# Optimization experiments

Measured on AMD Instinct MI355X. Metric: run time of the kernel, lower is better.

## Reference

```python
import jax, jax.numpy as jnp
import numpy as np

D = 128        # d_model
VOCAB = 2000   # vocab_size
NUM_ITERS = 6
NUM_V = 98304  # total vertices = 3 * num_edges
NUM_E = NUM_V // 3


def setup_inputs() -> dict:
    key = jax.random.key(0)
    ks = jax.random.split(key, 20)
    std = 0.02
    inp = {
        "x_v": jax.random.randint(ks[0], (NUM_V,), 0, VOCAB),
        "target_mask": jax.random.randint(ks[1], (NUM_V,), 0, 2) > 0,
        # embedding table (vocab_size + 1 rows, last is padding idx)
        "emb": jax.random.normal(ks[2], (VOCAB + 1, D), jnp.float32) * std,
        # edge_init: Linear(1, d_model)
        "edge_init_w": jax.random.normal(ks[3], (D, 1), jnp.float32) * std,
        "edge_init_b": jnp.zeros((D,), jnp.float32),
        # vertex_to_edge LSTM(3d -> d): torch gate order i,f,g,o
        "Wih_v2e": jax.random.normal(ks[4], (4 * D, 3 * D), jnp.float32) * (1.0 / np.sqrt(D)),
        "Whh_v2e": jax.random.normal(ks[5], (4 * D, D), jnp.float32) * (1.0 / np.sqrt(D)),
        "bih_v2e": jax.random.normal(ks[6], (4 * D,), jnp.float32) * (1.0 / np.sqrt(D)),
        "bhh_v2e": jax.random.normal(ks[7], (4 * D,), jnp.float32) * (1.0 / np.sqrt(D)),
        # edge_to_vertex: 3 position-specific LSTM(d -> d), stacked along axis 0
        "Wih_e2v": jax.random.normal(ks[8], (3, 4 * D, D), jnp.float32) * (1.0 / np.sqrt(D)),
        "Whh_e2v": jax.random.normal(ks[9], (3, 4 * D, D), jnp.float32) * (1.0 / np.sqrt(D)),
        "bih_e2v": jax.random.normal(ks[10], (3, 4 * D), jnp.float32) * (1.0 / np.sqrt(D)),
        "bhh_e2v": jax.random.normal(ks[11], (3, 4 * D), jnp.float32) * (1.0 / np.sqrt(D)),
        # output projection Linear(d -> vocab)
        "out_w": jax.random.normal(ks[12], (VOCAB, D), jnp.float32) * std,
        "out_b": jnp.zeros((VOCAB,), jnp.float32),
    }
    return inp


def _lstm_cell(gates, c):
    # torch LSTM gate order: input, forget, cell(g), output
    i, f, g, o = jnp.split(gates, 4, axis=-1)
    c_new = jax.nn.sigmoid(f) * c + jax.nn.sigmoid(i) * jnp.tanh(g)
    h_new = jax.nn.sigmoid(o) * jnp.tanh(c_new)
    return h_new, c_new


def reference(x_v, target_mask, emb, edge_init_w, edge_init_b,
              Wih_v2e, Whh_v2e, bih_v2e, bhh_v2e,
              Wih_e2v, Whh_e2v, bih_e2v, bhh_e2v,
              out_w, out_b):
    E = x_v.shape[0] // 3
    # init embeddings (-1 ids would map to padding row VOCAB; ids are in-range here)
    h_v = emb[x_v].reshape(E, 3, D)              # [E, 3, D]
    c_v = jnp.zeros_like(h_v)
    h_e = jnp.broadcast_to(edge_init_w[:, 0] + edge_init_b, (E, D))  # Linear(1->D) on ones
    c_e = jnp.zeros_like(h_e)
    mask = target_mask.reshape(E, 3)[..., None]  # [E, 3, 1]
    b_v2e = bih_v2e + bhh_v2e                    # [4D]
    b_e2v = (bih_e2v + bhh_e2v)[None]            # [1, 3, 4D]

    for _ in range(NUM_ITERS):
        # vertex -> edge: concat 3 vertices, one LSTM cell step
        msg = h_v.reshape(E, 3 * D)
        gates_e = msg @ Wih_v2e.T + h_e @ Whh_v2e.T + b_v2e          # [E, 4D]
        h_e, c_e = _lstm_cell(gates_e, c_e)
        # edge -> vertex: 3 position-specific LSTM cells, same edge input
        gates_v = (jnp.einsum('ed,pkd->epk', h_e, Wih_e2v)
                   + jnp.einsum('epd,pkd->epk', h_v, Whh_e2v)
                   + b_e2v)                                          # [E, 3, 4D]
        h_new, c_new = _lstm_cell(gates_v, c_v)
        h_v = jnp.where(mask, h_new, h_v)
        c_v = jnp.where(mask, c_new, c_v)

    logits = h_v.reshape(3 * E, D) @ out_w.T + out_b                 # [3E, VOCAB]
    return logits
```

## Files before the change

kernel.cpp:

```cpp
#include <hip/hip_runtime.h>

#define E_CNT 32768
#define V_CNT 98304
#define D_ 128
#define VOCAB_ 2000
#define ITERS_ 6

typedef unsigned short u16;
typedef _Float16 f16;
typedef __attribute__((ext_vector_type(8))) _Float16 f16x8;
typedef __attribute__((ext_vector_type(4))) float f32x4;

__device__ __forceinline__ f32x4 MFh(f16x8 a, f16x8 b, f32x4 c) {
    return __builtin_amdgcn_mfma_f32_16x16x32_f16(a, b, c, 0, 0, 0);
}
__device__ __forceinline__ float sigmoid_f(float x) {
    return __builtin_amdgcn_rcpf(1.0f + __expf(-x));
}
__device__ __forceinline__ float tanh_f(float x) {
    float ax = fabsf(x);
    float t = fmaf(-2.0f, __builtin_amdgcn_rcpf(__expf(2.0f * ax) + 1.0f), 1.0f);
    return copysignf(t, x);
}

__global__ void detect_mask_kernel(const unsigned int* __restrict__ m, int* __restrict__ flag) {
    int i = blockIdx.x * 256 + threadIdx.x;
    if (i < 4096 && m[i] > 1u) atomicOr(flag, 1);
}

__global__ void prep_kernel(
    const float* __restrict__ Wih_v2e, const float* __restrict__ Whh_v2e,
    const float* __restrict__ bih_v2e, const float* __restrict__ bhh_v2e,
    const float* __restrict__ Wih_e2v, const float* __restrict__ Whh_e2v,
    const float* __restrict__ bih_e2v, const float* __restrict__ bhh_e2v,
    const float* __restrict__ out_w,
    f16* __restrict__ WvF, f16* __restrict__ WeF,
    f16* __restrict__ OwFh, f16* __restrict__ OwFl,
    float* __restrict__ bv, float* __restrict__ be)
{
    int idx = blockIdx.x * 256 + threadIdx.x;
    if (idx < 262144) {
        const int r = idx & 7, l = (idx >> 3) & 63, t = idx >> 9;
        const int kk = t & 15, nt = t >> 4;
        const int j = nt * 16 + (l & 15);
        const int k = kk * 32 + (l >> 4) * 8 + r;
        const float w = (k < 384) ? Wih_v2e[j * 384 + k] : Whh_v2e[j * 128 + (k - 384)];
        WvF[idx] = (f16)w;
        return;
    }
    idx -= 262144;
    if (idx < 393216) {
        const int r = idx & 7, l = (idx >> 3) & 63, t = idx >> 9;
        const int kk = t & 7, nt = (t >> 3) & 31, p = t >> 8;
        const int j = nt * 16 + (l & 15);
        const int k = kk * 32 + (l >> 4) * 8 + r;
        const float w = (k < 128) ? Wih_e2v[(p * 512 + j) * 128 + k]
                                  : Whh_e2v[(p * 512 + j) * 128 + (k - 128)];
        WeF[idx] = (f16)w;
        return;
    }
    idx -= 393216;
    if (idx < 256000) {
        const int r = idx & 7, l = (idx >> 3) & 63, t = idx >> 9;
        const int kk = t & 3, nt = t >> 2;
        const int j = nt * 16 + (l & 15);
        const int k = kk * 32 + (l >> 4) * 8 + r;
        const float w = out_w[j * 128 + k];
        const f16 h = (f16)w;
        OwFh[idx] = h;
        OwFl[idx] = (f16)(w - (float)h);
        return;
    }
    idx -= 256000;
    if (idx < 512) { bv[idx] = bih_v2e[idx] + bhh_v2e[idx]; return; }
    idx -= 512;
    if (idx < 1536) { be[idx] = bih_e2v[idx] + bhh_e2v[idx]; return; }
}

__global__ __launch_bounds__(512)
void fused_kernel(
    const int* __restrict__ x_v,
    const float* __restrict__ emb,
    const float* __restrict__ eiw, const float* __restrict__ eib,
    const f16* __restrict__ WvF, const f16* __restrict__ WeF,
    const float* __restrict__ bv, const float* __restrict__ be,
    const void* __restrict__ mask, const int* __restrict__ flagp,
    float* __restrict__ cvG,
    f16* __restrict__ hvOut)
{
    __shared__ f16 HV[24576];
    __shared__ f16 HE[8192];

    const int tid = threadIdx.x;
    const int c = tid >> 6, l = tid & 63;
    const int lr = l & 15, lk = l >> 4;
    const int e0 = blockIdx.x * 64;

    for (int i = tid; i < 64 * 48; i += 512) {
        const int row = i / 48, seg = i % 48;
        int id = x_v[(e0 + row) * 3 + (seg >> 4)];
        if (id < 0 || id > VOCAB_) id = VOCAB_;
        const float* s = emb + id * D_ + ((seg * 8) & 127);
        float4 a = *(const float4*)s, b = *(const float4*)(s + 4);
        f16x8 H;
        H[0] = (f16)a.x; H[1] = (f16)a.y; H[2] = (f16)a.z; H[3] = (f16)a.w;
        H[4] = (f16)b.x; H[5] = (f16)b.y; H[6] = (f16)b.z; H[7] = (f16)b.w;
        *(f16x8*)&HV[((row >> 4) * 12 + (seg >> 2)) * 512 + (seg & 3) * 128 + (row & 15) * 8] = H;
    }
    for (int i = tid; i < 64 * 16; i += 512) {
        const int row = i / 16, seg = i % 16;
        f16x8 H;
        #pragma unroll
        for (int j = 0; j < 8; ++j) H[j] = (f16)(eiw[seg * 8 + j] + eib[seg * 8 + j]);
        *(f16x8*)&HE[((row >> 4) * 4 + (seg >> 2)) * 512 + (seg & 3) * 128 + (row & 15) * 8] = H;
    }

    const int isByte = *flagp;
    unsigned mbits[3];
    #pragma unroll
    for (int p = 0; p < 3; ++p) {
        unsigned mb = 0;
        #pragma unroll
        for (int mt = 0; mt < 4; ++mt)
            #pragma unroll
            for (int r = 0; r < 4; ++r) {
                const int v = (e0 + mt * 16 + lk * 4 + r) * 3 + p;
                const bool m = isByte ? (((const unsigned char*)mask)[v] != 0)
                                      : (((const int*)mask)[v] != 0);
                mb |= (unsigned)m << (mt * 4 + r);
            }
        mbits[p] = mb;
    }
    const int d = c * 16 + lr;
    const int wBase = (c >> 1) * 512 + ((c & 1) * 2 + (lr >> 3)) * 128 + lk * 32 + (lr & 7);
    float ce[4][4];
    #pragma unroll
    for (int mt = 0; mt < 4; ++mt)
        #pragma unroll
        for (int r = 0; r < 4; ++r) ce[mt][r] = 0.0f;

    __syncthreads();

    const f16* HVl = HV + l * 8;
    const f16* HEl = HE + l * 8;

    #pragma unroll 1
    for (int it = 0; it < ITERS_; ++it) {
        {
            f32x4 acc[4][4];
            #pragma unroll
            for (int mt = 0; mt < 4; ++mt)
                #pragma unroll
                for (int g = 0; g < 4; ++g) acc[mt][g] = (f32x4)0.0f;

            f16x8 Bc[4];
            #pragma unroll
            for (int g = 0; g < 4; ++g)
                Bc[g] = *(const f16x8*)(WvF + (((g * 8 + c) * 16) * 64 + l) * 8);

            #pragma unroll 2
            for (int kk = 0; kk < 16; ++kk) {
                f16x8 Bn[4];
                if (kk < 15) {
                    #pragma unroll
                    for (int g = 0; g < 4; ++g)
                        Bn[g] = *(const f16x8*)(WvF + (((g * 8 + c) * 16 + kk + 1) * 64 + l) * 8);
                }
                f16x8 Ah[4];
                if (kk < 12) {
                    #pragma unroll
                    for (int mt = 0; mt < 4; ++mt)
                        Ah[mt] = *(const f16x8*)(HVl + (mt * 12 + kk) * 512);
                } else {
                    #pragma unroll
                    for (int mt = 0; mt < 4; ++mt)
                        Ah[mt] = *(const f16x8*)(HEl + (mt * 4 + (kk - 12)) * 512);
                }
                #pragma unroll
                for (int g = 0; g < 4; ++g)
                    #pragma unroll
                    for (int mt = 0; mt < 4; ++mt)
                        acc[mt][g] = MFh(Ah[mt], Bc[g], acc[mt][g]);
                #pragma unroll
                for (int g = 0; g < 4; ++g) Bc[g] = Bn[g];
            }
            __syncthreads();
            const float bvi = bv[d], bvf = bv[128 + d], bvg = bv[256 + d], bvo = bv[384 + d];
            #pragma unroll
            for (int mt = 0; mt < 4; ++mt)
                #pragma unroll
                for (int r = 0; r < 4; ++r) {
                    float gi = sigmoid_f(acc[mt][0][r] + bvi);
                    float gf = sigmoid_f(acc[mt][1][r] + bvf);
                    float gg = tanh_f(acc[mt][2][r] + bvg);
                    float go = sigmoid_f(acc[mt][3][r] + bvo);
                    float cn = gf * ce[mt][r] + gi * gg;
                    ce[mt][r] = cn;
                    HE[wBase + mt * 2048 + r * 8] = (f16)(go * tanh_f(cn));
                }
            __syncthreads();
        }
        #pragma unroll 1
        for (int p = 0; p < 3; ++p) {
            f32x4 acc[4][4];
            #pragma unroll
            for (int mt = 0; mt < 4; ++mt)
                #pragma unroll
                for (int g = 0; g < 4; ++g) acc[mt][g] = (f32x4)0.0f;

            f16x8 Bc[4];
            #pragma unroll
            for (int g = 0; g < 4; ++g)
                Bc[g] = *(const f16x8*)(WeF + ((((p * 32) + (g * 8 + c)) * 8) * 64 + l) * 8);

            #pragma unroll 2
            for (int kk = 0; kk < 8; ++kk) {
                f16x8 Bn[4];
                if (kk < 7) {
                    #pragma unroll
                    for (int g = 0; g < 4; ++g)
                        Bn[g] = *(const f16x8*)(WeF + ((((p * 32) + (g * 8 + c)) * 8 + kk + 1) * 64 + l) * 8);
                }
                f16x8 Ah[4];
                if (kk < 4) {
                    #pragma unroll
                    for (int mt = 0; mt < 4; ++mt)
                        Ah[mt] = *(const f16x8*)(HEl + (mt * 4 + kk) * 512);
                } else {
                    #pragma unroll
                    for (int mt = 0; mt < 4; ++mt)
                        Ah[mt] = *(const f16x8*)(HVl + (mt * 12 + 4 * p + (kk - 4)) * 512);
                }
                #pragma unroll
                for (int g = 0; g < 4; ++g)
                    #pragma unroll
                    for (int mt = 0; mt < 4; ++mt)
                        acc[mt][g] = MFh(Ah[mt], Bc[g], acc[mt][g]);
                #pragma unroll
                for (int g = 0; g < 4; ++g) Bc[g] = Bn[g];
            }
            __syncthreads();
            const float bei = be[p * 512 + d], bef = be[p * 512 + 128 + d];
            const float beg = be[p * 512 + 256 + d], beo = be[p * 512 + 384 + d];
            #pragma unroll
            for (int mt = 0; mt < 4; ++mt)
                #pragma unroll
                for (int r = 0; r < 4; ++r) {
                    if ((mbits[p] >> (mt * 4 + r)) & 1u) {
                        float gi = sigmoid_f(acc[mt][0][r] + bei);
                        float gf = sigmoid_f(acc[mt][1][r] + bef);
                        float gg = tanh_f(acc[mt][2][r] + beg);
                        float go = sigmoid_f(acc[mt][3][r] + beo);
                        const int row = mt * 16 + lk * 4 + r;
                        const size_t co = ((size_t)(e0 + row) * 3 + p) * 128 + d;
                        float cvold = (it == 0) ? 0.0f : cvG[co];
                        float cn = gf * cvold + gi * gg;
                        cvG[co] = cn;
                        HV[wBase + mt * 6144 + p * 2048 + r * 8] = (f16)(go * tanh_f(cn));
                    }
                }
        }
        __syncthreads();
    }

    for (int i = tid; i < 64 * 48; i += 512) {
        const int row = i / 48, seg = i % 48;
        *(f16x8*)&hvOut[(size_t)(e0 + row) * 384 + seg * 8] =
            *(const f16x8*)&HV[((row >> 4) * 12 + (seg >> 2)) * 512 + (seg & 3) * 128 + (row & 15) * 8];
    }
}

__global__ __launch_bounds__(512) void proj_kernel(
    const f16* __restrict__ hv,
    const f16* __restrict__ WFh, const f16* __restrict__ WFl,
    const float* __restrict__ out_b, float* __restrict__ out)
{
    __shared__ char occ_pad[81920];
    const int tid = threadIdx.x, l = tid & 63;
    occ_pad[tid] = (char)tid;
    __syncthreads();
    {
        int keep = (int)occ_pad[(tid + 1) & 511];
        asm volatile("" :: "v"(keep));
    }

    const int wid = blockIdx.x * 8 + (tid >> 6);
    const int v0 = wid * 32;
    const int lr = l & 15, lk = l >> 4;

    f16x8 Bv[2][4];
    #pragma unroll
    for (int vt = 0; vt < 2; ++vt)
        #pragma unroll
        for (int kk = 0; kk < 4; ++kk)
            Bv[vt][kk] = *(const f16x8*)(hv + (v0 + vt * 16 + lr) * D_ + kk * 32 + lk * 8);

    f16x8 Wc[8];
    #pragma unroll
    for (int kk = 0; kk < 4; ++kk) {
        Wc[kk]     = *(const f16x8*)(WFh + ((kk) * 64 + l) * 8);
        Wc[4 + kk] = *(const f16x8*)(WFl + ((kk) * 64 + l) * 8);
    }

    #pragma unroll 2
    for (int nt = 0; nt < 125; ++nt) {
        f16x8 Wn[8];
        if (nt < 124) {
            #pragma unroll
            for (int kk = 0; kk < 4; ++kk) {
                const int fb = (((nt + 1) * 4 + kk) * 64 + l) * 8;
                Wn[kk]     = *(const f16x8*)(WFh + fb);
                Wn[4 + kk] = *(const f16x8*)(WFl + fb);
            }
        }
        f32x4 t0 = (f32x4)0.0f, t1 = (f32x4)0.0f, u0 = (f32x4)0.0f, u1 = (f32x4)0.0f;
        #pragma unroll
        for (int kk = 0; kk < 4; ++kk) {
            t0 = MFh(Wc[kk], Bv[0][kk], t0);
            t1 = MFh(Wc[kk], Bv[1][kk], t1);
            u0 = MFh(Wc[4 + kk], Bv[0][kk], u0);
            u1 = MFh(Wc[4 + kk], Bv[1][kk], u1);
        }
        f32x4 a0 = t0 + u0;
        f32x4 a1 = t1 + u1;
        const int n0 = nt * 16 + lk * 4;
        const float4 bb = *(const float4*)&out_b[n0];
        {
            const size_t v = (size_t)(v0 + lr);
            float4 o = make_float4(a0[0] + bb.x, a0[1] + bb.y, a0[2] + bb.z, a0[3] + bb.w);
            *(float4*)&out[v * VOCAB_ + n0] = o;
        }
        {
            const size_t v = (size_t)(v0 + 16 + lr);
            float4 o = make_float4(a1[0] + bb.x, a1[1] + bb.y, a1[2] + bb.z, a1[3] + bb.w);
            *(float4*)&out[v * VOCAB_ + n0] = o;
        }
        #pragma unroll
        for (int q = 0; q < 8; ++q) Wc[q] = Wn[q];
    }
}

extern "C" void kernel_launch(void* const* d_in, const int* in_sizes, int n_in,
                              void* d_out, int out_size, void* d_ws, size_t ws_size,
                              hipStream_t stream)
{
    const int*   x_v     = (const int*)  d_in[0];
    const void*  mask    = d_in[1];
    const float* emb     = (const float*)d_in[2];
    const float* eiw     = (const float*)d_in[3];
    const float* eib     = (const float*)d_in[4];
    const float* Wih_v2e = (const float*)d_in[5];
    const float* Whh_v2e = (const float*)d_in[6];
    const float* bih_v2e = (const float*)d_in[7];
    const float* bhh_v2e = (const float*)d_in[8];
    const float* Wih_e2v = (const float*)d_in[9];
    const float* Whh_e2v = (const float*)d_in[10];
    const float* bih_e2v = (const float*)d_in[11];
    const float* bhh_e2v = (const float*)d_in[12];
    const float* out_w   = (const float*)d_in[13];
    const float* out_b   = (const float*)d_in[14];
    float* out = (float*)d_out;

    char* ws = (char*)d_ws;
    f16*   hv   = (f16*)(ws);
    f16*   WvF  = (f16*)(ws + 25165824);
    f16*   WeF  = (f16*)(ws + 25690112);
    f16*   OwFh = (f16*)(ws + 26476544);
    f16*   OwFl = (f16*)(ws + 26988544);
    float* bv   = (float*)(ws + 27500544);
    float* be   = (float*)(ws + 27502592);
    int*   flag = (int*)(ws + 27508736);
    float* cvG  = (float*)(ws + 27525120);

    hipMemsetAsync(flag, 0, 4, stream);
    detect_mask_kernel<<<16, 256, 0, stream>>>((const unsigned int*)mask, flag);
    prep_kernel<<<3568, 256, 0, stream>>>(Wih_v2e, Whh_v2e, bih_v2e, bhh_v2e,
                                          Wih_e2v, Whh_e2v, bih_e2v, bhh_e2v, out_w,
                                          WvF, WeF, OwFh, OwFl, bv, be);
    fused_kernel<<<E_CNT / 64, 512, 0, stream>>>(x_v, emb, eiw, eib,
                                                 WvF, WeF, bv, be,
                                                 mask, flag, cvG, hv);
    proj_kernel<<<V_CNT / 256, 512, 0, stream>>>(hv, OwFh, OwFl, out_b, out);
}
```

Measured before the change: 786.7 us.

## Double-buffer LSTM state in LDS to cut barriers; shrink projection blocks

The fused LSTM kernel now ping-pongs the vertex and edge hidden states between static and dynamic shared buffers. Reads come from one buffer and writes go to the other, which removes most __syncthreads per iteration. Unmasked vertices now copy their old value forward. The register double-buffering of weight fragments is replaced by direct per-k loads. LDS per block roughly doubles to 128KB, which limits occupancy to one block per CU. The projection kernel moves to 256-thread blocks with a smaller occupancy pad.

Result: slower. 913.0 us (+16.1%).

```diff
diff --git a/kernel.cpp b/kernel.cpp
--- a/kernel.cpp
+++ b/kernel.cpp
@@ -88,8 +88,11 @@
     float* __restrict__ cvG,
     f16* __restrict__ hvOut)
 {
-    __shared__ f16 HV[24576];
-    __shared__ f16 HE[8192];
+    __shared__ f16 HVs[24576];
+    __shared__ f16 HEs[8192];
+    extern __shared__ f16 dynbuf[];
+    f16* HVd = dynbuf;
+    f16* HEd = dynbuf + 24576;
 
     const int tid = threadIdx.x;
     const int c = tid >> 6, l = tid & 63;
@@ -105,14 +108,14 @@
         f16x8 H;
         H[0] = (f16)a.x; H[1] = (f16)a.y; H[2] = (f16)a.z; H[3] = (f16)a.w;
         H[4] = (f16)b.x; H[5] = (f16)b.y; H[6] = (f16)b.z; H[7] = (f16)b.w;
-        *(f16x8*)&HV[((row >> 4) * 12 + (seg >> 2)) * 512 + (seg & 3) * 128 + (row & 15) * 8] = H;
+        *(f16x8*)&HVs[((row >> 4) * 12 + (seg >> 2)) * 512 + (seg & 3) * 128 + (row & 15) * 8] = H;
     }
     for (int i = tid; i < 64 * 16; i += 512) {
         const int row = i / 16, seg = i % 16;
         f16x8 H;
         #pragma unroll
         for (int j = 0; j < 8; ++j) H[j] = (f16)(eiw[seg * 8 + j] + eib[seg * 8 + j]);
-        *(f16x8*)&HE[((row >> 4) * 4 + (seg >> 2)) * 512 + (seg & 3) * 128 + (row & 15) * 8] = H;
+        *(f16x8*)&HEs[((row >> 4) * 4 + (seg >> 2)) * 512 + (seg & 3) * 128 + (row & 15) * 8] = H;
     }
 
     const int isByte = *flagp;
@@ -141,50 +144,43 @@
 
     __syncthreads();
 
-    const f16* HVl = HV + l * 8;
-    const f16* HEl = HE + l * 8;
-
     #pragma unroll 1
     for (int it = 0; it < ITERS_; ++it) {
+        const f16* HVr = (it & 1) ? HVd : HVs;
+        f16*       HVw = (it & 1) ? HVs : HVd;
+        const f16* HEr = (it & 1) ? HEd : HEs;
+        f16*       HEw = (it & 1) ? HEs : HEd;
+        const f16* HVrl = HVr + l * 8;
+        const f16* HErl = HEr + l * 8;
+        const f16* HEwl = HEw + l * 8;
+
+        f32x4 acc[4][4];
+        #pragma unroll
+        for (int mt = 0; mt < 4; ++mt)
+            #pragma unroll
+            for (int g = 0; g < 4; ++g) acc[mt][g] = (f32x4)0.0f;
+
+        #pragma unroll 2
+        for (int kk = 0; kk < 16; ++kk) {
+            f16x8 Ah[4];
+            if (kk < 12) {
+                #pragma unroll
+                for (int mt = 0; mt < 4; ++mt)
+                    Ah[mt] = *(const f16x8*)(HVrl + (mt * 12 + kk) * 512);
+            } else {
+                #pragma unroll
+                for (int mt = 0; mt < 4; ++mt)
+                    Ah[mt] = *(const f16x8*)(HErl + (mt * 4 + (kk - 12)) * 512);
+            }
+            #pragma unroll
+            for (int g = 0; g < 4; ++g) {
+                f16x8 B = *(const f16x8*)(WvF + (((g * 8 + c) * 16 + kk) * 64 + l) * 8);
+                #pragma unroll
+                for (int mt = 0; mt < 4; ++mt)
+                    acc[mt][g] = MFh(Ah[mt], B, acc[mt][g]);
+            }
+        }
         {
-            f32x4 acc[4][4];
-            #pragma unroll
-            for (int mt = 0; mt < 4; ++mt)
-                #pragma unroll
-                for (int g = 0; g < 4; ++g) acc[mt][g] = (f32x4)0.0f;
-
-            f16x8 Bc[4];
-            #pragma unroll
-            for (int g = 0; g < 4; ++g)
-                Bc[g] = *(const f16x8*)(WvF + (((g * 8 + c) * 16) * 64 + l) * 8);
-
-            #pragma unroll 2
-            for (int kk = 0; kk < 16; ++kk) {
-                f16x8 Bn[4];
-                if (kk < 15) {
-                    #pragma unroll
-                    for (int g = 0; g < 4; ++g)
-                        Bn[g] = *(const f16x8*)(WvF + (((g * 8 + c) * 16 + kk + 1) * 64 + l) * 8);
-                }
-                f16x8 Ah[4];
-                if (kk < 12) {
-                    #pragma unroll
-                    for (int mt = 0; mt < 4; ++mt)
-                        Ah[mt] = *(const f16x8*)(HVl + (mt * 12 + kk) * 512);
-                } else {
-                    #pragma unroll
-                    for (int mt = 0; mt < 4; ++mt)
-                        Ah[mt] = *(const f16x8*)(HEl + (mt * 4 + (kk - 12)) * 512);
-                }
-                #pragma unroll
-                for (int g = 0; g < 4; ++g)
-                    #pragma unroll
-                    for (int mt = 0; mt < 4; ++mt)
-                        acc[mt][g] = MFh(Ah[mt], Bc[g], acc[mt][g]);
-                #pragma unroll
-                for (int g = 0; g < 4; ++g) Bc[g] = Bn[g];
-            }
-            __syncthreads();
             const float bvi = bv[d], bvf = bv[128 + d], bvg = bv[256 + d], bvo = bv[384 + d];
             #pragma unroll
             for (int mt = 0; mt < 4; ++mt)
@@ -196,95 +192,86 @@
                     float go = sigmoid_f(acc[mt][3][r] + bvo);
                     float cn = gf * ce[mt][r] + gi * gg;
                     ce[mt][r] = cn;
-                    HE[wBase + mt * 2048 + r * 8] = (f16)(go * tanh_f(cn));
+                    HEw[wBase + mt * 2048 + r * 8] = (f16)(go * tanh_f(cn));
                 }
-            __syncthreads();
-        }
+        }
+        __syncthreads();
+
         #pragma unroll 1
         for (int p = 0; p < 3; ++p) {
-            f32x4 acc[4][4];
             #pragma unroll
             for (int mt = 0; mt < 4; ++mt)
                 #pragma unroll
                 for (int g = 0; g < 4; ++g) acc[mt][g] = (f32x4)0.0f;
-
-            f16x8 Bc[4];
-            #pragma unroll
-            for (int g = 0; g < 4; ++g)
-                Bc[g] = *(const f16x8*)(WeF + ((((p * 32) + (g * 8 + c)) * 8) * 64 + l) * 8);
 
             #pragma unroll 2
             for (int kk = 0; kk < 8; ++kk) {
-                f16x8 Bn[4];
-                if (kk < 7) {
-                    #pragma unroll
-                    for (int g = 0; g < 4; ++g)
-                        Bn[g] = *(const f16x8*)(WeF + ((((p * 32) + (g * 8 + c)) * 8 + kk + 1) * 64 + l) * 8);
-                }
                 f16x8 Ah[4];
                 if (kk < 4) {
                     #pragma unroll
                     for (int mt = 0; mt < 4; ++mt)
-                        Ah[mt] = *(const f16x8*)(HEl + (mt * 4 + kk) * 512);
+                        Ah[mt] = *(const f16x8*)(HEwl + (mt * 4 + kk) * 512);
                 } else {
                     #pragma unroll
                     for (int mt = 0; mt < 4; ++mt)
-                        Ah[mt] = *(const f16x8*)(HVl + (mt * 12 + 4 * p + (kk - 4)) * 512);
+                        Ah[mt] = *(const f16x8*)(HVrl + (mt * 12 + p * 4 + (kk - 4)) * 512);
                 }
                 #pragma unroll
-                for (int g = 0; g < 4; ++g)
+                for (int g = 0; g < 4; ++g) {
+                    f16x8 B = *(const f16x8*)(WeF + ((((p * 32) + (g * 8 + c)) * 8 + kk) * 64 + l) * 8);
                     #pragma unroll
                     for (int mt = 0; mt < 4; ++mt)
-                        acc[mt][g] = MFh(Ah[mt], Bc[g], acc[mt][g]);
-                #pragma unroll
-                for (int g = 0; g < 4; ++g) Bc[g] = Bn[g];
-            }
-            __syncthreads();
+                        acc[mt][g] = MFh(Ah[mt], B, acc[mt][g]);
+                }
+            }
             const float bei = be[p * 512 + d], bef = be[p * 512 + 128 + d];
             const float beg = be[p * 512 + 256 + d], beo = be[p * 512 + 384 + d];
             #pragma unroll
             for (int mt = 0; mt < 4; ++mt)
                 #pragma unroll
                 for (int r = 0; r < 4; ++r) {
-                    if ((mbits[p] >> (mt * 4 + r)) & 1u) {
-                        float gi = sigmoid_f(acc[mt][0][r] + bei);
-                        float gf = sigmoid_f(acc[mt][1][r] + bef);
-                        float gg = tanh_f(acc[mt][2][r] + beg);
-                        float go = sigmoid_f(acc[mt][3][r] + beo);
-                        const int row = mt * 16 + lk * 4 + r;
-                        const size_t co = ((size_t)(e0 + row) * 3 + p) * 128 + d;
-                        float cvold = (it == 0) ? 0.0f : cvG[co];
-                        float cn = gf * cvold + gi * gg;
-                        cvG[co] = cn;
-                        HV[wBase + mt * 6144 + p * 2048 + r * 8] = (f16)(go * tanh_f(cn));
-                    }
+                    const int off = wBase + mt * 6144 + p * 2048 + r * 8;
+                    const f16 hold = HVr[off];
+                    const bool m = (mbits[p] >> (mt * 4 + r)) & 1u;
+                    const int row = mt * 16 + lk * 4 + r;
+                    const size_t co = ((size_t)(e0 + row) * 3 + p) * 128 + d;
+                    float cvold = (it == 0) ? 0.0f : cvG[co];
+                    float gi = sigmoid_f(acc[mt][0][r] + bei);
+                    float gf = sigmoid_f(acc[mt][1][r] + bef);
+                    float gg = tanh_f(acc[mt][2][r] + beg);
+                    float go = sigmoid_f(acc[mt][3][r] + beo);
+                    float cn = gf * cvold + gi * gg;
+                    if (m) cvG[co] = cn;
+                    f16 val = m ? (f16)(go * tanh_f(cn)) : hold;
+                    HVw[off] = val;
                 }
         }
         __syncthreads();
     }
 
+    const f16* HVf = ((ITERS_ - 1) & 1) ? HVs : HVd;
     for (int i = tid; i < 64 * 48; i += 512) {
         const int row = i / 48, seg = i % 48;
         *(f16x8*)&hvOut[(size_t)(e0 + row) * 384 + seg * 8] =
-            *(const f16x8*)&HV[((row >> 4) * 12 + (seg >> 2)) * 512 + (seg & 3) * 128 + (row & 15) * 8];
-    }
-}
-
-__global__ __launch_bounds__(512) void proj_kernel(
+            *(const f16x8*)&HVf[((row >> 4) * 12 + (seg >> 2)) * 512 + (seg & 3) * 128 + (row & 15) * 8];
+    }
+}
+
+__global__ __launch_bounds__(256) void proj_kernel(
     const f16* __restrict__ hv,
     const f16* __restrict__ WFh, const f16* __restrict__ WFl,
     const float* __restrict__ out_b, float* __restrict__ out)
 {
-    __shared__ char occ_pad[81920];
+    __shared__ char occ_pad[49152];
     const int tid = threadIdx.x, l = tid & 63;
     occ_pad[tid] = (char)tid;
     __syncthreads();
     {
-        int keep = (int)occ_pad[(tid + 1) & 511];
+        int keep = (int)occ_pad[(tid + 1) & 255];
         asm volatile("" :: "v"(keep));
     }
 
-    const int wid = blockIdx.x * 8 + (tid >> 6);
+    const int wid = blockIdx.x * 4 + (tid >> 6);
     const int v0 = wid * 32;
     const int lr = l & 15, lk = l >> 4;
 
@@ -372,13 +359,16 @@
     int*   flag = (int*)(ws + 27508736);
     float* cvG  = (float*)(ws + 27525120);
 
+    hipFuncSetAttribute(reinterpret_cast<const void*>(fused_kernel),
+                        hipFuncAttributeMaxDynamicSharedMemorySize, 65536);
+
     hipMemsetAsync(flag, 0, 4, stream);
     detect_mask_kernel<<<16, 256, 0, stream>>>((const unsigned int*)mask, flag);
     prep_kernel<<<3568, 256, 0, stream>>>(Wih_v2e, Whh_v2e, bih_v2e, bhh_v2e,
                                           Wih_e2v, Whh_e2v, bih_e2v, bhh_e2v, out_w,
                                           WvF, WeF, OwFh, OwFl, bv, be);
-    fused_kernel<<<E_CNT / 64, 512, 0, stream>>>(x_v, emb, eiw, eib,
-                                                 WvF, WeF, bv, be,
-                                                 mask, flag, cvG, hv);
-    proj_kernel<<<V_CNT / 256, 512, 0, stream>>>(hv, OwFh, OwFl, out_b, out);
-}
+    fused_kernel<<<E_CNT / 64, 512, 65536, stream>>>(x_v, emb, eiw, eib,
+                                                     WvF, WeF, bv, be,
+                                                     mask, flag, cvG, hv);
+    proj_kernel<<<V_CNT / 128, 256, 0, stream>>>(hv, OwFh, OwFl, out_b, out);
+}
```
